# Kernel optimization log

Hardware: AMD Instinct MI355X
Metric: run time of the kernel (lower is better)

## Reference

```python
import jax, jax.numpy as jnp
import numpy as np

B, H, S, D = 4, 16, 2048, 64
MASK_FILL = 1e-12  # module quirk: masked scores set to 1e-12, not -inf


def setup_inputs() -> dict:
    key = jax.random.key(0)
    kq, kk, kv, km = jax.random.split(key, 4)
    q = jax.random.normal(kq, (B, H, S, D), dtype=jnp.float32)
    k = jax.random.normal(kk, (B, H, S, D), dtype=jnp.float32)
    v = jax.random.normal(kv, (B, H, S, D), dtype=jnp.float32)
    mask = jax.random.randint(km, (B, 1, 1, S), 0, 2, dtype=jnp.int32)
    return {"q": q, "k": k, "v": v, "mask": mask}


def reference(q, k, v, mask):
    dim = k.shape[-1]
    # scores: [B,H,S,S]
    scores = jnp.einsum('bhid,bhjd->bhij', q, k) * (dim ** -0.5)
    # faithful to masked_fill(mask == 0, 1e-12)
    scores = jnp.where(mask == 0, jnp.asarray(MASK_FILL, scores.dtype), scores)
    attention = jax.nn.softmax(scores, axis=-1)
    output = jnp.einsum('bhij,bhjd->bhid', attention, v)
    return output, attention
```

## Files before the change

### kernel.cpp

```cpp
#include <hip/hip_runtime.h>
#include <hip/hip_bf16.h>

namespace {

constexpr int S = 2048;
constexpr int D = 64;
constexpr int NT = S / 32;
constexpr float QSCALE = 0.125f * 1.4426950408889634f;

typedef __bf16 bf16x8 __attribute__((ext_vector_type(8)));
typedef float f32x16 __attribute__((ext_vector_type(16)));
typedef unsigned int uint32x4 __attribute__((ext_vector_type(4)));

#if __has_builtin(__builtin_amdgcn_exp2f)
__device__ __forceinline__ float fexp2(float x) { return __builtin_amdgcn_exp2f(x); }
#else
__device__ __forceinline__ float fexp2(float x) { return exp2f(x); }
#endif

__device__ __forceinline__ bf16x8 cvt8s(float4 a, float4 b, float s) {
    bf16x8 f;
    f[0] = (__bf16)(a.x * s); f[1] = (__bf16)(a.y * s);
    f[2] = (__bf16)(a.z * s); f[3] = (__bf16)(a.w * s);
    f[4] = (__bf16)(b.x * s); f[5] = (__bf16)(b.y * s);
    f[6] = (__bf16)(b.z * s); f[7] = (__bf16)(b.w * s);
    return f;
}
__device__ __forceinline__ bf16x8 cvt8(float4 a, float4 b) {
    bf16x8 f;
    f[0] = (__bf16)a.x; f[1] = (__bf16)a.y;
    f[2] = (__bf16)a.z; f[3] = (__bf16)a.w;
    f[4] = (__bf16)b.x; f[5] = (__bf16)b.y;
    f[6] = (__bf16)b.z; f[7] = (__bf16)b.w;
    return f;
}
__device__ __forceinline__ unsigned int pkbf(float lo, float hi) {
    unsigned int a = (unsigned int)__builtin_bit_cast(unsigned short, (__bf16)lo);
    unsigned int b = (unsigned int)__builtin_bit_cast(unsigned short, (__bf16)hi);
    return a | (b << 16);
}

}

__global__ void __launch_bounds__(256, 4)
attn_fused(const float* __restrict__ qg, const float* __restrict__ kg,
           const float* __restrict__ vg, const int* __restrict__ mg,
           float* __restrict__ og, float* __restrict__ ag)
{
    __shared__ bf16x8 kstage[3][256];
    __shared__ bf16x8 vstage[3][256];
    __shared__ unsigned int mlds[64];

    const int tid  = threadIdx.x;
    const int lane = tid & 63;
    const int w    = tid >> 6;
    const int l31  = lane & 31;
    const int h2   = lane >> 5;

    const int wid = (blockIdx.x & 7) * 128 + (blockIdx.x >> 3);
    const int bh  = wid >> 4;
    const int q0  = ((wid & 15) * 4 + w) * 32;
    const int b   = bh >> 4;

    const float* qrow = qg + ((size_t)bh * S + q0 + l31) * D + 8 * h2;
    const float* vb_  = vg + (size_t)bh * S * D;
    float* att  = ag + (size_t)bh * S * S + (size_t)q0 * S;
    float* orow = og + ((size_t)bh * S + q0) * D;

    const int srow  = tid >> 3;
    const int scol  = tid & 7;
    const int sslot = srow * 8 + (scol ^ (srow & 7));
    const float* ksrc = kg + (size_t)bh * S * D + (size_t)srow * D + scol * 8;
    int kslot[4];
#pragma unroll
    for (int t = 0; t < 4; ++t)
        kslot[t] = l31 * 8 + ((2 * t + h2) ^ (l31 & 7));

    const int vd = tid & 63;
    const int vw = tid >> 6;
    const int vwslot = vd * 4 + (vw ^ ((vd >> 1) & 3));
    const float* vsrc = vb_ + vd;
    int vslot[2][2];
#pragma unroll
    for (int f = 0; f < 2; ++f)
#pragma unroll
        for (int g = 0; g < 2; ++g) {
            const int d = l31 + 32 * g;
            vslot[f][g] = d * 4 + ((2 * f + h2) ^ ((d >> 1) & 3));
        }

    bf16x8 qa[4];
#pragma unroll
    for (int t = 0; t < 4; ++t) {
        const float4* p4 = (const float4*)(qrow + 16 * t);
        qa[t] = cvt8s(p4[0], p4[1], QSCALE);
    }

    if (tid < 64) {
        const int4* mp = (const int4*)(mg + (size_t)b * S + 32 * tid);
        unsigned int bits = 0;
#pragma unroll
        for (int k = 0; k < 8; ++k) {
            int4 m = mp[k];
            bits |= (unsigned int)(m.x != 0) << (4 * k);
            bits |= (unsigned int)(m.y != 0) << (4 * k + 1);
            bits |= (unsigned int)(m.z != 0) << (4 * k + 2);
            bits |= (unsigned int)(m.w != 0) << (4 * k + 3);
        }
        mlds[tid] = bits;
    }

    {
        const float4* p4 = (const float4*)ksrc;
        kstage[0][sslot] = cvt8(p4[0], p4[1]);
        bf16x8 vv;
#pragma unroll
        for (int k = 0; k < 8; ++k)
            vv[k] = (__bf16)vsrc[(size_t)(8 * vw + k) * D];
        vstage[0][vwslot] = vv;
    }
    float4 k1a, k1b;
    float  v1[8];
    {
        const float4* p4 = (const float4*)(ksrc + (size_t)32 * D);
        k1a = p4[0]; k1b = p4[1];
#pragma unroll
        for (int k = 0; k < 8; ++k)
            v1[k] = vsrc[(size_t)(32 + 8 * vw + k) * D];
    }
    __syncthreads();

    float sums4[4] = {0.f, 0.f, 0.f, 0.f};
    f32x16 oacc[2];
#pragma unroll
    for (int g = 0; g < 2; ++g)
#pragma unroll
        for (int r = 0; r < 16; ++r) oacc[g][r] = 0.f;

    int cur = 0;
    for (int t = 0; t < NT; ++t) {
        const int j0  = t * 32;
        const int nxt = (cur == 2) ? 0 : cur + 1;

        float4 k2a{}, k2b{};
        float  v2[8];
        const bool have2 = (t + 2) < NT;
        if (have2) {
            const float4* p4 = (const float4*)(ksrc + (size_t)(j0 + 64) * D);
            k2a = p4[0]; k2b = p4[1];
#pragma unroll
            for (int k = 0; k < 8; ++k)
                v2[k] = vsrc[(size_t)(j0 + 64 + 8 * vw + k) * D];
        }

        f32x16 acc;
#pragma unroll
        for (int r = 0; r < 16; ++r) acc[r] = 0.f;
        __builtin_amdgcn_s_setprio(1);
#pragma unroll
        for (int u = 0; u < 4; ++u)
            acc = __builtin_amdgcn_mfma_f32_32x32x16_bf16(kstage[cur][kslot[u]], qa[u], acc, 0, 0, 0);
        __builtin_amdgcn_s_setprio(0);

        const unsigned int mq = mlds[j0 >> 5] >> (4 * h2);
        unsigned int pk[8];
#pragma unroll
        for (int qd = 0; qd < 4; ++qd) {
            float pv[4];
#pragma unroll
            for (int i = 0; i < 4; ++i) {
                const float e = fexp2(acc[4 * qd + i]);
                pv[i] = ((mq >> (i + 8 * qd)) & 1) ? e : 1.0f;
                sums4[qd] += pv[i];
            }
            pk[2 * qd]     = pkbf(pv[0], pv[1]);
            pk[2 * qd + 1] = pkbf(pv[2], pv[3]);
        }
        asm volatile("v_permlane32_swap_b32 %0, %1" : "+v"(pk[0]), "+v"(pk[2]));
        asm volatile("v_permlane32_swap_b32 %0, %1" : "+v"(pk[1]), "+v"(pk[3]));
        asm volatile("v_permlane32_swap_b32 %0, %1" : "+v"(pk[4]), "+v"(pk[6]));
        asm volatile("v_permlane32_swap_b32 %0, %1" : "+v"(pk[5]), "+v"(pk[7]));
        uint32x4 u0 = {pk[0], pk[1], pk[2], pk[3]};
        uint32x4 u1 = {pk[4], pk[5], pk[6], pk[7]};
        bf16x8 pa[2];
        pa[0] = __builtin_bit_cast(bf16x8, u0);
        pa[1] = __builtin_bit_cast(bf16x8, u1);

        __builtin_amdgcn_s_setprio(1);
#pragma unroll
        for (int f = 0; f < 2; ++f)
#pragma unroll
            for (int g = 0; g < 2; ++g)
                oacc[g] = __builtin_amdgcn_mfma_f32_32x32x16_bf16(pa[f], vstage[cur][vslot[f][g]], oacc[g], 0, 0, 0);
        __builtin_amdgcn_s_setprio(0);

        if ((t + 1) < NT) {
            kstage[nxt][sslot] = cvt8(k1a, k1b);
            bf16x8 vv;
#pragma unroll
            for (int k = 0; k < 8; ++k) vv[k] = (__bf16)v1[k];
            vstage[nxt][vwslot] = vv;
        }
        __syncthreads();

        k1a = k2a; k1b = k2b;
#pragma unroll
        for (int k = 0; k < 8; ++k) v1[k] = v2[k];
        cur = nxt;
    }

    const float ssum = (sums4[0] + sums4[1]) + (sums4[2] + sums4[3]);
    const float inv = 1.0f / (ssum + __shfl_xor(ssum, 32));
    float invq[16];
#pragma unroll
    for (int r = 0; r < 16; ++r)
        invq[r] = __shfl(inv, (r & 3) + 8 * (r >> 2) + 4 * h2);

#pragma unroll
    for (int g = 0; g < 2; ++g)
#pragma unroll
        for (int r = 0; r < 16; ++r) {
            const int qr = (r & 3) + 8 * (r >> 2) + 4 * h2;
            __builtin_nontemporal_store(oacc[g][r] * invq[r],
                                        &orow[(size_t)qr * D + 32 * g + l31]);
        }

    {
        const float4* p4 = (const float4*)ksrc;
        kstage[0][sslot] = cvt8(p4[0], p4[1]);
    }
    __syncthreads();

    cur = 0;
    for (int j0 = 0; j0 < S; j0 += 32) {
        const bool more = (j0 + 32) < S;
        float4 kna{}, knb{};
        if (more) {
            const float4* p4 = (const float4*)(ksrc + (size_t)(j0 + 32) * D);
            kna = p4[0]; knb = p4[1];
        }
        const bool mf = (mlds[j0 >> 5] >> l31) & 1;

        f32x16 acc;
#pragma unroll
        for (int r = 0; r < 16; ++r) acc[r] = 0.f;
        __builtin_amdgcn_s_setprio(1);
#pragma unroll
        for (int u = 0; u < 4; ++u)
            acc = __builtin_amdgcn_mfma_f32_32x32x16_bf16(qa[u], kstage[cur][kslot[u]], acc, 0, 0, 0);
        __builtin_amdgcn_s_setprio(0);

#pragma unroll
        for (int r = 0; r < 16; ++r) {
            float p = mf ? fexp2(acc[r]) : 1.0f;
            p *= invq[r];
            const int qr = (r & 3) + 8 * (r >> 2) + 4 * h2;
            __builtin_nontemporal_store(p, &att[(size_t)qr * S + j0 + l31]);
        }
        if (more) kstage[cur ^ 1][sslot] = cvt8(kna, knb);
        __syncthreads();
        cur ^= 1;
    }
}

extern "C" void kernel_launch(void* const* d_in, const int* in_sizes, int n_in,
                              void* d_out, int out_size, void* d_ws, size_t ws_size,
                              hipStream_t stream) {
    const float* q    = (const float*)d_in[0];
    const float* k    = (const float*)d_in[1];
    const float* v    = (const float*)d_in[2];
    const int*   mask = (const int*)d_in[3];
    float* out = (float*)d_out;
    float* att = out + (size_t)64 * S * D;
    hipLaunchKernelGGL(attn_fused, dim3(1024), dim3(256), 0, stream,
                       q, k, v, mask, out, att);
}
```

Measured before the change: 289.6 us.

## Pre-convert K/V to bf16 workspace with cooperative grid sync before attention

```diff
diff --git a/kernel.cpp b/kernel.cpp
--- a/kernel.cpp
+++ b/kernel.cpp
@@ -1,5 +1,8 @@
 #include <hip/hip_runtime.h>
 #include <hip/hip_bf16.h>
+#include <hip/hip_cooperative_groups.h>
+
+namespace cg = cooperative_groups;
 
 namespace {
 
@@ -43,9 +46,10 @@
 }
 
 __global__ void __launch_bounds__(256, 4)
-attn_fused(const float* __restrict__ qg, const float* __restrict__ kg,
-           const float* __restrict__ vg, const int* __restrict__ mg,
-           float* __restrict__ og, float* __restrict__ ag)
+attn_coop(const float* __restrict__ qg, const float* __restrict__ kg,
+          const float* __restrict__ vg, const int* __restrict__ mg,
+          float* __restrict__ og, float* __restrict__ ag,
+          unsigned short* __restrict__ kb, unsigned short* __restrict__ vt)
 {
     __shared__ bf16x8 kstage[3][256];
     __shared__ bf16x8 vstage[3][256];
@@ -62,15 +66,42 @@
     const int q0  = ((wid & 15) * 4 + w) * 32;
     const int b   = bh >> 4;
 
+    {
+        const int slice = wid & 15;
+        const float* kgh = kg + (size_t)bh * S * D;
+        const float* vgh = vg + (size_t)bh * S * D;
+        unsigned short* kbh = kb + (size_t)bh * S * D;
+        unsigned short* vth = vt + (size_t)bh * S * D;
+#pragma unroll
+        for (int r = 0; r < 4; ++r) {
+            const int row = slice * 128 + r * 32 + (tid >> 3);
+            const int c8  = (tid & 7) * 8;
+            const float4* src = (const float4*)(kgh + (size_t)row * D + c8);
+            *(bf16x8*)(kbh + (size_t)row * D + c8) = cvt8(src[0], src[1]);
+        }
+        const int dcol = tid & 63;
+        const int jblk = tid >> 6;
+#pragma unroll
+        for (int c = 0; c < 4; ++c) {
+            const int j = slice * 128 + jblk * 32 + c * 8;
+            bf16x8 vv;
+#pragma unroll
+            for (int kk = 0; kk < 8; ++kk)
+                vv[kk] = (__bf16)vgh[(size_t)(j + kk) * D + dcol];
+            *(bf16x8*)(vth + (size_t)dcol * S + j) = vv;
+        }
+    }
+    __threadfence();
+    cg::this_grid().sync();
+
     const float* qrow = qg + ((size_t)bh * S + q0 + l31) * D + 8 * h2;
-    const float* vb_  = vg + (size_t)bh * S * D;
     float* att  = ag + (size_t)bh * S * S + (size_t)q0 * S;
     float* orow = og + ((size_t)bh * S + q0) * D;
 
     const int srow  = tid >> 3;
     const int scol  = tid & 7;
     const int sslot = srow * 8 + (scol ^ (srow & 7));
-    const float* ksrc = kg + (size_t)bh * S * D + (size_t)srow * D + scol * 8;
+    const unsigned short* ksrc = kb + (size_t)bh * S * D + (size_t)srow * D + scol * 8;
     int kslot[4];
 #pragma unroll
     for (int t = 0; t < 4; ++t)
@@ -79,7 +110,7 @@
     const int vd = tid & 63;
     const int vw = tid >> 6;
     const int vwslot = vd * 4 + (vw ^ ((vd >> 1) & 3));
-    const float* vsrc = vb_ + vd;
+    const unsigned short* vsrc = vt + (size_t)bh * S * D + (size_t)vd * S + 8 * vw;
     int vslot[2][2];
 #pragma unroll
     for (int f = 0; f < 2; ++f)
@@ -111,23 +142,15 @@
     }
 
     {
-        const float4* p4 = (const float4*)ksrc;
-        kstage[0][sslot] = cvt8(p4[0], p4[1]);
-        bf16x8 vv;
-#pragma unroll
-        for (int k = 0; k < 8; ++k)
-            vv[k] = (__bf16)vsrc[(size_t)(8 * vw + k) * D];
-        vstage[0][vwslot] = vv;
-    }
-    float4 k1a, k1b;
-    float  v1[8];
-    {
-        const float4* p4 = (const float4*)(ksrc + (size_t)32 * D);
-        k1a = p4[0]; k1b = p4[1];
-#pragma unroll
-        for (int k = 0; k < 8; ++k)
-            v1[k] = vsrc[(size_t)(32 + 8 * vw + k) * D];
-    }
+        uint32x4 ku, vu;
+        __builtin_memcpy(&ku, ksrc, 16);
+        __builtin_memcpy(&vu, vsrc, 16);
+        kstage[0][sslot]  = __builtin_bit_cast(bf16x8, ku);
+        vstage[0][vwslot] = __builtin_bit_cast(bf16x8, vu);
+    }
+    uint32x4 k1, v1;
+    __builtin_memcpy(&k1, ksrc + (size_t)32 * D, 16);
+    __builtin_memcpy(&v1, vsrc + 32, 16);
     __syncthreads();
 
     float sums4[4] = {0.f, 0.f, 0.f, 0.f};
@@ -142,15 +165,10 @@
         const int j0  = t * 32;
         const int nxt = (cur == 2) ? 0 : cur + 1;
 
-        float4 k2a{}, k2b{};
-        float  v2[8];
-        const bool have2 = (t + 2) < NT;
-        if (have2) {
-            const float4* p4 = (const float4*)(ksrc + (size_t)(j0 + 64) * D);
-            k2a = p4[0]; k2b = p4[1];
-#pragma unroll
-            for (int k = 0; k < 8; ++k)
-                v2[k] = vsrc[(size_t)(j0 + 64 + 8 * vw + k) * D];
+        uint32x4 k2{}, v2{};
+        if ((t + 2) < NT) {
+            __builtin_memcpy(&k2, ksrc + (size_t)(j0 + 64) * D, 16);
+            __builtin_memcpy(&v2, vsrc + (j0 + 64), 16);
         }
 
         f32x16 acc;
@@ -195,6 +213,221 @@
         __builtin_amdgcn_s_setprio(0);
 
         if ((t + 1) < NT) {
+            kstage[nxt][sslot]  = __builtin_bit_cast(bf16x8, k1);
+            vstage[nxt][vwslot] = __builtin_bit_cast(bf16x8, v1);
+        }
+        __syncthreads();
+
+        k1 = k2; v1 = v2;
+        cur = nxt;
+    }
+
+    const float ssum = (sums4[0] + sums4[1]) + (sums4[2] + sums4[3]);
+    const float inv = 1.0f / (ssum + __shfl_xor(ssum, 32));
+    float invq[16];
+#pragma unroll
+    for (int r = 0; r < 16; ++r)
+        invq[r] = __shfl(inv, (r & 3) + 8 * (r >> 2) + 4 * h2);
+
+#pragma unroll
+    for (int g = 0; g < 2; ++g)
+#pragma unroll
+        for (int r = 0; r < 16; ++r) {
+            const int qr = (r & 3) + 8 * (r >> 2) + 4 * h2;
+            __builtin_nontemporal_store(oacc[g][r] * invq[r],
+                                        &orow[(size_t)qr * D + 32 * g + l31]);
+        }
+
+    {
+        uint32x4 ku;
+        __builtin_memcpy(&ku, ksrc, 16);
+        kstage[0][sslot] = __builtin_bit_cast(bf16x8, ku);
+    }
+    __syncthreads();
+
+    cur = 0;
+    for (int j0 = 0; j0 < S; j0 += 32) {
+        const bool more = (j0 + 32) < S;
+        uint32x4 kn{};
+        if (more)
+            __builtin_memcpy(&kn, ksrc + (size_t)(j0 + 32) * D, 16);
+        const bool mf = (mlds[j0 >> 5] >> l31) & 1;
+
+        f32x16 acc;
+#pragma unroll
+        for (int r = 0; r < 16; ++r) acc[r] = 0.f;
+        __builtin_amdgcn_s_setprio(1);
+#pragma unroll
+        for (int u = 0; u < 4; ++u)
+            acc = __builtin_amdgcn_mfma_f32_32x32x16_bf16(qa[u], kstage[cur][kslot[u]], acc, 0, 0, 0);
+        __builtin_amdgcn_s_setprio(0);
+
+#pragma unroll
+        for (int r = 0; r < 16; ++r) {
+            float p = mf ? fexp2(acc[r]) : 1.0f;
+            p *= invq[r];
+            const int qr = (r & 3) + 8 * (r >> 2) + 4 * h2;
+            __builtin_nontemporal_store(p, &att[(size_t)qr * S + j0 + l31]);
+        }
+        if (more) kstage[cur ^ 1][sslot] = __builtin_bit_cast(bf16x8, kn);
+        __syncthreads();
+        cur ^= 1;
+    }
+}
+
+__global__ void __launch_bounds__(256, 4)
+attn_fused(const float* __restrict__ qg, const float* __restrict__ kg,
+           const float* __restrict__ vg, const int* __restrict__ mg,
+           float* __restrict__ og, float* __restrict__ ag)
+{
+    __shared__ bf16x8 kstage[3][256];
+    __shared__ bf16x8 vstage[3][256];
+    __shared__ unsigned int mlds[64];
+
+    const int tid  = threadIdx.x;
+    const int lane = tid & 63;
+    const int w    = tid >> 6;
+    const int l31  = lane & 31;
+    const int h2   = lane >> 5;
+
+    const int wid = (blockIdx.x & 7) * 128 + (blockIdx.x >> 3);
+    const int bh  = wid >> 4;
+    const int q0  = ((wid & 15) * 4 + w) * 32;
+    const int b   = bh >> 4;
+
+    const float* qrow = qg + ((size_t)bh * S + q0 + l31) * D + 8 * h2;
+    const float* vb_  = vg + (size_t)bh * S * D;
+    float* att  = ag + (size_t)bh * S * S + (size_t)q0 * S;
+    float* orow = og + ((size_t)bh * S + q0) * D;
+
+    const int srow  = tid >> 3;
+    const int scol  = tid & 7;
+    const int sslot = srow * 8 + (scol ^ (srow & 7));
+    const float* ksrc = kg + (size_t)bh * S * D + (size_t)srow * D + scol * 8;
+    int kslot[4];
+#pragma unroll
+    for (int t = 0; t < 4; ++t)
+        kslot[t] = l31 * 8 + ((2 * t + h2) ^ (l31 & 7));
+
+    const int vd = tid & 63;
+    const int vw = tid >> 6;
+    const int vwslot = vd * 4 + (vw ^ ((vd >> 1) & 3));
+    const float* vsrc = vb_ + vd;
+    int vslot[2][2];
+#pragma unroll
+    for (int f = 0; f < 2; ++f)
+#pragma unroll
+        for (int g = 0; g < 2; ++g) {
+            const int d = l31 + 32 * g;
+            vslot[f][g] = d * 4 + ((2 * f + h2) ^ ((d >> 1) & 3));
+        }
+
+    bf16x8 qa[4];
+#pragma unroll
+    for (int t = 0; t < 4; ++t) {
+        const float4* p4 = (const float4*)(qrow + 16 * t);
+        qa[t] = cvt8s(p4[0], p4[1], QSCALE);
+    }
+
+    if (tid < 64) {
+        const int4* mp = (const int4*)(mg + (size_t)b * S + 32 * tid);
+        unsigned int bits = 0;
+#pragma unroll
+        for (int k = 0; k < 8; ++k) {
+            int4 m = mp[k];
+            bits |= (unsigned int)(m.x != 0) << (4 * k);
+            bits |= (unsigned int)(m.y != 0) << (4 * k + 1);
+            bits |= (unsigned int)(m.z != 0) << (4 * k + 2);
+            bits |= (unsigned int)(m.w != 0) << (4 * k + 3);
+        }
+        mlds[tid] = bits;
+    }
+
+    {
+        const float4* p4 = (const float4*)ksrc;
+        kstage[0][sslot] = cvt8(p4[0], p4[1]);
+        bf16x8 vv;
+#pragma unroll
+        for (int k = 0; k < 8; ++k)
+            vv[k] = (__bf16)vsrc[(size_t)(8 * vw + k) * D];
+        vstage[0][vwslot] = vv;
+    }
+    float4 k1a, k1b;
+    float  v1[8];
+    {
+        const float4* p4 = (const float4*)(ksrc + (size_t)32 * D);
+        k1a = p4[0]; k1b = p4[1];
+#pragma unroll
+        for (int k = 0; k < 8; ++k)
+            v1[k] = vsrc[(size_t)(32 + 8 * vw + k) * D];
+    }
+    __syncthreads();
+
+    float sums4[4] = {0.f, 0.f, 0.f, 0.f};
+    f32x16 oacc[2];
+#pragma unroll
+    for (int g = 0; g < 2; ++g)
+#pragma unroll
+        for (int r = 0; r < 16; ++r) oacc[g][r] = 0.f;
+
+    int cur = 0;
+    for (int t = 0; t < NT; ++t) {
+        const int j0  = t * 32;
+        const int nxt = (cur == 2) ? 0 : cur + 1;
+
+        float4 k2a{}, k2b{};
+        float  v2[8];
+        const bool have2 = (t + 2) < NT;
+        if (have2) {
+            const float4* p4 = (const float4*)(ksrc + (size_t)(j0 + 64) * D);
+            k2a = p4[0]; k2b = p4[1];
+#pragma unroll
+            for (int k = 0; k < 8; ++k)
+                v2[k] = vsrc[(size_t)(j0 + 64 + 8 * vw + k) * D];
+        }
+
+        f32x16 acc;
+#pragma unroll
+        for (int r = 0; r < 16; ++r) acc[r] = 0.f;
+        __builtin_amdgcn_s_setprio(1);
+#pragma unroll
+        for (int u = 0; u < 4; ++u)
+            acc = __builtin_amdgcn_mfma_f32_32x32x16_bf16(kstage[cur][kslot[u]], qa[u], acc, 0, 0, 0);
+        __builtin_amdgcn_s_setprio(0);
+
+        const unsigned int mq = mlds[j0 >> 5] >> (4 * h2);
+        unsigned int pk[8];
+#pragma unroll
+        for (int qd = 0; qd < 4; ++qd) {
+            float pv[4];
+#pragma unroll
+            for (int i = 0; i < 4; ++i) {
+                const float e = fexp2(acc[4 * qd + i]);
+                pv[i] = ((mq >> (i + 8 * qd)) & 1) ? e : 1.0f;
+                sums4[qd] += pv[i];
+            }
+            pk[2 * qd]     = pkbf(pv[0], pv[1]);
+            pk[2 * qd + 1] = pkbf(pv[2], pv[3]);
+        }
+        asm volatile("v_permlane32_swap_b32 %0, %1" : "+v"(pk[0]), "+v"(pk[2]));
+        asm volatile("v_permlane32_swap_b32 %0, %1" : "+v"(pk[1]), "+v"(pk[3]));
+        asm volatile("v_permlane32_swap_b32 %0, %1" : "+v"(pk[4]), "+v"(pk[6]));
+        asm volatile("v_permlane32_swap_b32 %0, %1" : "+v"(pk[5]), "+v"(pk[7]));
+        uint32x4 u0 = {pk[0], pk[1], pk[2], pk[3]};
+        uint32x4 u1 = {pk[4], pk[5], pk[6], pk[7]};
+        bf16x8 pa[2];
+        pa[0] = __builtin_bit_cast(bf16x8, u0);
+        pa[1] = __builtin_bit_cast(bf16x8, u1);
+
+        __builtin_amdgcn_s_setprio(1);
+#pragma unroll
+        for (int f = 0; f < 2; ++f)
+#pragma unroll
+            for (int g = 0; g < 2; ++g)
+                oacc[g] = __builtin_amdgcn_mfma_f32_32x32x16_bf16(pa[f], vstage[cur][vslot[f][g]], oacc[g], 0, 0, 0);
+        __builtin_amdgcn_s_setprio(0);
+
+        if ((t + 1) < NT) {
             kstage[nxt][sslot] = cvt8(k1a, k1b);
             bf16x8 vv;
 #pragma unroll
@@ -272,6 +505,22 @@
     const int*   mask = (const int*)d_in[3];
     float* out = (float*)d_out;
     float* att = out + (size_t)64 * S * D;
-    hipLaunchKernelGGL(attn_fused, dim3(1024), dim3(256), 0, stream,
-                       q, k, v, mask, out, att);
-}
+
+    const size_t kv_elems = (size_t)64 * S * D;
+    const size_t kv_bytes = kv_elems * sizeof(unsigned short);
+    bool done = false;
+    if (ws_size >= 2 * kv_bytes) {
+        unsigned short* kb = (unsigned short*)d_ws;
+        unsigned short* vt = kb + kv_elems;
+        void* args[] = {(void*)&q, (void*)&k, (void*)&v, (void*)&mask,
+                        (void*)&out, (void*)&att, (void*)&kb, (void*)&vt};
+        hipError_t e = hipLaunchCooperativeKernel((void*)attn_coop,
+                                                  dim3(1024), dim3(256),
+                                                  args, 0, stream);
+        done = (e == hipSuccess);
+    }
+    if (!done) {
+        hipLaunchKernelGGL(attn_fused, dim3(1024), dim3(256), 0, stream,
+                           q, k, v, mask, out, att);
+    }
+}
```

Measured after the change: 542.3 us. +87.3%, slower.

## Process two 32-row query tiles per wave to reuse staged K/V fragments

Applied to the files above, without the earlier changes.

```diff
diff --git a/kernel.cpp b/kernel.cpp
--- a/kernel.cpp
+++ b/kernel.cpp
@@ -42,7 +42,7 @@
 
 }
 
-__global__ void __launch_bounds__(256, 4)
+__global__ void __launch_bounds__(256, 2)
 attn_fused(const float* __restrict__ qg, const float* __restrict__ kg,
            const float* __restrict__ vg, const int* __restrict__ mg,
            float* __restrict__ og, float* __restrict__ ag)
@@ -57,12 +57,11 @@
     const int l31  = lane & 31;
     const int h2   = lane >> 5;
 
-    const int wid = (blockIdx.x & 7) * 128 + (blockIdx.x >> 3);
-    const int bh  = wid >> 4;
-    const int q0  = ((wid & 15) * 4 + w) * 32;
+    const int wid = (blockIdx.x & 7) * 64 + (blockIdx.x >> 3);
+    const int bh  = wid >> 3;
+    const int q0  = ((wid & 7) * 4 + w) * 64;
     const int b   = bh >> 4;
 
-    const float* qrow = qg + ((size_t)bh * S + q0 + l31) * D + 8 * h2;
     const float* vb_  = vg + (size_t)bh * S * D;
     float* att  = ag + (size_t)bh * S * S + (size_t)q0 * S;
     float* orow = og + ((size_t)bh * S + q0) * D;
@@ -89,11 +88,15 @@
             vslot[f][g] = d * 4 + ((2 * f + h2) ^ ((d >> 1) & 3));
         }
 
-    bf16x8 qa[4];
-#pragma unroll
-    for (int t = 0; t < 4; ++t) {
-        const float4* p4 = (const float4*)(qrow + 16 * t);
-        qa[t] = cvt8s(p4[0], p4[1], QSCALE);
+    bf16x8 qa[2][4];
+#pragma unroll
+    for (int s = 0; s < 2; ++s) {
+        const float* qrow = qg + ((size_t)bh * S + q0 + 32 * s + l31) * D + 8 * h2;
+#pragma unroll
+        for (int t = 0; t < 4; ++t) {
+            const float4* p4 = (const float4*)(qrow + 16 * t);
+            qa[s][t] = cvt8s(p4[0], p4[1], QSCALE);
+        }
     }
 
     if (tid < 64) {
@@ -130,12 +133,14 @@
     }
     __syncthreads();
 
-    float sums4[4] = {0.f, 0.f, 0.f, 0.f};
-    f32x16 oacc[2];
-#pragma unroll
-    for (int g = 0; g < 2; ++g)
-#pragma unroll
-        for (int r = 0; r < 16; ++r) oacc[g][r] = 0.f;
+    float sums4[2][4] = {{0.f, 0.f, 0.f, 0.f}, {0.f, 0.f, 0.f, 0.f}};
+    f32x16 oacc[2][2];
+#pragma unroll
+    for (int s = 0; s < 2; ++s)
+#pragma unroll
+        for (int g = 0; g < 2; ++g)
+#pragma unroll
+            for (int r = 0; r < 16; ++r) oacc[s][g][r] = 0.f;
 
     int cur = 0;
     for (int t = 0; t < NT; ++t) {
@@ -144,8 +149,7 @@
 
         float4 k2a{}, k2b{};
         float  v2[8];
-        const bool have2 = (t + 2) < NT;
-        if (have2) {
+        if ((t + 2) < NT) {
             const float4* p4 = (const float4*)(ksrc + (size_t)(j0 + 64) * D);
             k2a = p4[0]; k2b = p4[1];
 #pragma unroll
@@ -153,46 +157,59 @@
                 v2[k] = vsrc[(size_t)(j0 + 64 + 8 * vw + k) * D];
         }
 
-        f32x16 acc;
-#pragma unroll
-        for (int r = 0; r < 16; ++r) acc[r] = 0.f;
-        __builtin_amdgcn_s_setprio(1);
-#pragma unroll
-        for (int u = 0; u < 4; ++u)
-            acc = __builtin_amdgcn_mfma_f32_32x32x16_bf16(kstage[cur][kslot[u]], qa[u], acc, 0, 0, 0);
-        __builtin_amdgcn_s_setprio(0);
+        bf16x8 kf[4];
+#pragma unroll
+        for (int u = 0; u < 4; ++u) kf[u] = kstage[cur][kslot[u]];
+        bf16x8 vf[2][2];
+#pragma unroll
+        for (int f = 0; f < 2; ++f)
+#pragma unroll
+            for (int g = 0; g < 2; ++g) vf[f][g] = vstage[cur][vslot[f][g]];
 
         const unsigned int mq = mlds[j0 >> 5] >> (4 * h2);
-        unsigned int pk[8];
-#pragma unroll
-        for (int qd = 0; qd < 4; ++qd) {
-            float pv[4];
-#pragma unroll
-            for (int i = 0; i < 4; ++i) {
-                const float e = fexp2(acc[4 * qd + i]);
-                pv[i] = ((mq >> (i + 8 * qd)) & 1) ? e : 1.0f;
-                sums4[qd] += pv[i];
+
+#pragma unroll
+        for (int s = 0; s < 2; ++s) {
+            f32x16 acc;
+#pragma unroll
+            for (int r = 0; r < 16; ++r) acc[r] = 0.f;
+            __builtin_amdgcn_s_setprio(1);
+#pragma unroll
+            for (int u = 0; u < 4; ++u)
+                acc = __builtin_amdgcn_mfma_f32_32x32x16_bf16(kf[u], qa[s][u], acc, 0, 0, 0);
+            __builtin_amdgcn_s_setprio(0);
+
+            unsigned int pk[8];
+#pragma unroll
+            for (int qd = 0; qd < 4; ++qd) {
+                float pv[4];
+#pragma unroll
+                for (int i = 0; i < 4; ++i) {
+                    const float e = fexp2(acc[4 * qd + i]);
+                    pv[i] = ((mq >> (i + 8 * qd)) & 1) ? e : 1.0f;
+                    sums4[s][qd] += pv[i];
+                }
+                pk[2 * qd]     = pkbf(pv[0], pv[1]);
+                pk[2 * qd + 1] = pkbf(pv[2], pv[3]);
             }
-            pk[2 * qd]     = pkbf(pv[0], pv[1]);
-            pk[2 * qd + 1] = pkbf(pv[2], pv[3]);
-        }
-        asm volatile("v_permlane32_swap_b32 %0, %1" : "+v"(pk[0]), "+v"(pk[2]));
-        asm volatile("v_permlane32_swap_b32 %0, %1" : "+v"(pk[1]), "+v"(pk[3]));
-        asm volatile("v_permlane32_swap_b32 %0, %1" : "+v"(pk[4]), "+v"(pk[6]));
-        asm volatile("v_permlane32_swap_b32 %0, %1" : "+v"(pk[5]), "+v"(pk[7]));
-        uint32x4 u0 = {pk[0], pk[1], pk[2], pk[3]};
-        uint32x4 u1 = {pk[4], pk[5], pk[6], pk[7]};
-        bf16x8 pa[2];
-        pa[0] = __builtin_bit_cast(bf16x8, u0);
-        pa[1] = __builtin_bit_cast(bf16x8, u1);
-
-        __builtin_amdgcn_s_setprio(1);
-#pragma unroll
-        for (int f = 0; f < 2; ++f)
-#pragma unroll
-            for (int g = 0; g < 2; ++g)
-                oacc[g] = __builtin_amdgcn_mfma_f32_32x32x16_bf16(pa[f], vstage[cur][vslot[f][g]], oacc[g], 0, 0, 0);
-        __builtin_amdgcn_s_setprio(0);
+            asm volatile("v_permlane32_swap_b32 %0, %1" : "+v"(pk[0]), "+v"(pk[2]));
+            asm volatile("v_permlane32_swap_b32 %0, %1" : "+v"(pk[1]), "+v"(pk[3]));
+            asm volatile("v_permlane32_swap_b32 %0, %1" : "+v"(pk[4]), "+v"(pk[6]));
+            asm volatile("v_permlane32_swap_b32 %0, %1" : "+v"(pk[5]), "+v"(pk[7]));
+            uint32x4 u0 = {pk[0], pk[1], pk[2], pk[3]};
+            uint32x4 u1 = {pk[4], pk[5], pk[6], pk[7]};
+            bf16x8 pa[2];
+            pa[0] = __builtin_bit_cast(bf16x8, u0);
+            pa[1] = __builtin_bit_cast(bf16x8, u1);
+
+            __builtin_amdgcn_s_setprio(1);
+#pragma unroll
+            for (int f = 0; f < 2; ++f)
+#pragma unroll
+                for (int g = 0; g < 2; ++g)
+                    oacc[s][g] = __builtin_amdgcn_mfma_f32_32x32x16_bf16(pa[f], vf[f][g], oacc[s][g], 0, 0, 0);
+            __builtin_amdgcn_s_setprio(0);
+        }
 
         if ((t + 1) < NT) {
             kstage[nxt][sslot] = cvt8(k1a, k1b);
@@ -209,21 +226,23 @@
         cur = nxt;
     }
 
-    const float ssum = (sums4[0] + sums4[1]) + (sums4[2] + sums4[3]);
-    const float inv = 1.0f / (ssum + __shfl_xor(ssum, 32));
-    float invq[16];
-#pragma unroll
-    for (int r = 0; r < 16; ++r)
-        invq[r] = __shfl(inv, (r & 3) + 8 * (r >> 2) + 4 * h2);
-
-#pragma unroll
-    for (int g = 0; g < 2; ++g)
-#pragma unroll
-        for (int r = 0; r < 16; ++r) {
-            const int qr = (r & 3) + 8 * (r >> 2) + 4 * h2;
-            __builtin_nontemporal_store(oacc[g][r] * invq[r],
-                                        &orow[(size_t)qr * D + 32 * g + l31]);
-        }
+    float invq[2][16];
+#pragma unroll
+    for (int s = 0; s < 2; ++s) {
+        const float ssum = (sums4[s][0] + sums4[s][1]) + (sums4[s][2] + sums4[s][3]);
+        const float inv = 1.0f / (ssum + __shfl_xor(ssum, 32));
+#pragma unroll
+        for (int r = 0; r < 16; ++r)
+            invq[s][r] = __shfl(inv, (r & 3) + 8 * (r >> 2) + 4 * h2);
+#pragma unroll
+        for (int g = 0; g < 2; ++g)
+#pragma unroll
+            for (int r = 0; r < 16; ++r) {
+                const int qr = 32 * s + (r & 3) + 8 * (r >> 2) + 4 * h2;
+                __builtin_nontemporal_store(oacc[s][g][r] * invq[s][r],
+                                            &orow[(size_t)qr * D + 32 * g + l31]);
+            }
+    }
 
     {
         const float4* p4 = (const float4*)ksrc;
@@ -241,21 +260,28 @@
         }
         const bool mf = (mlds[j0 >> 5] >> l31) & 1;
 
-        f32x16 acc;
-#pragma unroll
-        for (int r = 0; r < 16; ++r) acc[r] = 0.f;
-        __builtin_amdgcn_s_setprio(1);
-#pragma unroll
-        for (int u = 0; u < 4; ++u)
-            acc = __builtin_amdgcn_mfma_f32_32x32x16_bf16(qa[u], kstage[cur][kslot[u]], acc, 0, 0, 0);
-        __builtin_amdgcn_s_setprio(0);
-
-#pragma unroll
-        for (int r = 0; r < 16; ++r) {
-            float p = mf ? fexp2(acc[r]) : 1.0f;
-            p *= invq[r];
-            const int qr = (r & 3) + 8 * (r >> 2) + 4 * h2;
-            __builtin_nontemporal_store(p, &att[(size_t)qr * S + j0 + l31]);
+        bf16x8 kf[4];
+#pragma unroll
+        for (int u = 0; u < 4; ++u) kf[u] = kstage[cur][kslot[u]];
+
+#pragma unroll
+        for (int s = 0; s < 2; ++s) {
+            f32x16 acc;
+#pragma unroll
+            for (int r = 0; r < 16; ++r) acc[r] = 0.f;
+            __builtin_amdgcn_s_setprio(1);
+#pragma unroll
+            for (int u = 0; u < 4; ++u)
+                acc = __builtin_amdgcn_mfma_f32_32x32x16_bf16(qa[s][u], kf[u], acc, 0, 0, 0);
+            __builtin_amdgcn_s_setprio(0);
+
+#pragma unroll
+            for (int r = 0; r < 16; ++r) {
+                float p = mf ? fexp2(acc[r]) : 1.0f;
+                p *= invq[s][r];
+                const int qr = 32 * s + (r & 3) + 8 * (r >> 2) + 4 * h2;
+                __builtin_nontemporal_store(p, &att[(size_t)qr * S + j0 + l31]);
+            }
         }
         if (more) kstage[cur ^ 1][sslot] = cvt8(kna, knb);
         __syncthreads();
@@ -272,6 +298,6 @@
     const int*   mask = (const int*)d_in[3];
     float* out = (float*)d_out;
     float* att = out + (size_t)64 * S * D;
-    hipLaunchKernelGGL(attn_fused, dim3(1024), dim3(256), 0, stream,
+    hipLaunchKernelGGL(attn_fused, dim3(512), dim3(256), 0, stream,
                        q, k, v, mask, out, att);
 }
```

Result: no change. 294.7 us (+1.8%).
